# Optimization experiments

Measured on AMD Instinct MI355X. Metric: run time of the kernel, lower is better.

Reference implementation:

```python
import jax, jax.numpy as jnp
import numpy as np

EPS = 1e-5  # torch BatchNorm1d default eps


def setup_inputs() -> dict:
    key = jax.random.key(0)
    ks = jax.random.split(key, 12)
    B, D, H, R, T = 262144, 128, 64, 32, 8
    return {
        "x": jax.random.normal(ks[0], (B, D), dtype=jnp.float32),
        "t": jax.random.randint(ks[1], (B,), 0, T),
        # shared feature net: Linear(D->H), ReLU, BN(H) [eval mode], Dropout(eval=identity)
        "fw": jax.random.normal(ks[2], (H, D), dtype=jnp.float32) * 0.05,
        "fb": jax.random.normal(ks[3], (H,), dtype=jnp.float32) * 0.05,
        "f_gamma": jnp.ones((H,), jnp.float32),
        "f_beta": jnp.zeros((H,), jnp.float32),
        "f_mean": jax.random.normal(ks[4], (H,), dtype=jnp.float32) * 0.05,
        "f_var": jax.random.uniform(ks[5], (H,), minval=0.5, maxval=1.5),
        # T treatment heads, weights stacked on leading axis:
        # Linear(H->R), ReLU, BN(R), Dropout, Linear(R->1)
        "tw1": jax.random.normal(ks[6], (T, R, H), dtype=jnp.float32) * 0.05,
        "tb1": jax.random.normal(ks[7], (T, R), dtype=jnp.float32) * 0.05,
        "t_gamma": jnp.ones((T, R), jnp.float32),
        "t_beta": jnp.zeros((T, R), jnp.float32),
        "t_mean": jax.random.normal(ks[8], (T, R), dtype=jnp.float32) * 0.05,
        "t_var": jax.random.uniform(ks[9], (T, R), minval=0.5, maxval=1.5),
        "tw2": jax.random.normal(ks[10], (T, R), dtype=jnp.float32) * 0.05,  # [T,1,R] squeezed
        "tb2": jax.random.normal(ks[11], (T,), dtype=jnp.float32) * 0.05,
    }


def reference(x, t, fw, fb, f_gamma, f_beta, f_mean, f_var,
              tw1, tb1, t_gamma, t_beta, t_mean, t_var, tw2, tb2):
    # shared representation: Linear -> ReLU -> BN(eval) -> Dropout(identity)
    h = jax.nn.relu(x @ fw.T + fb)                                     # [B,H]
    h = f_gamma * (h - f_mean) * jax.lax.rsqrt(f_var + EPS) + f_beta   # [B,H]
    # run all T tiny heads densely, then select per-sample head (jit-friendly
    # equivalent of the boolean-mask gather/scatter loop; BN is eval-mode so
    # per-group masking and full-batch compute give identical math)
    z = jnp.einsum('bh,trh->btr', h, tw1) + tb1[None]                  # [B,T,R]
    z = jax.nn.relu(z)
    z = t_gamma[None] * (z - t_mean[None]) * jax.lax.rsqrt(t_var[None] + EPS) + t_beta[None]
    out_all = jnp.einsum('btr,tr->bt', z, tw2) + tb2[None]             # [B,T]
    pred = jnp.take_along_axis(out_all, t[:, None], axis=1)            # [B,1]
    return pred
```

## Files before the change

### kernel.cpp

```cpp
#include <hip/hip_runtime.h>
#include <hip/hip_bf16.h>
#include <cstdint>

#define EPS 1e-5f

typedef short bf16x8 __attribute__((ext_vector_type(8)));
typedef float f32x16 __attribute__((ext_vector_type(16)));
typedef unsigned int u32x4 __attribute__((ext_vector_type(4)));

#define WS_TW1S 0
#define WS_FWQ  8192
#define WS_TB1Q 12288
#define WS_W2Q  12544
#define WS_FBQ  12800
#define WS_C2   12864
#define WS_TOTAL 12872

static __device__ __forceinline__ unsigned short f2bf(float f) {
    unsigned int u = __float_as_uint(f);
    u += 0x7fffu + ((u >> 16) & 1u);
    return (unsigned short)(u >> 16);
}
static __device__ __forceinline__ unsigned pk_bf16(float lo, float hi) {
    unsigned l = (unsigned)(unsigned short)__builtin_bit_cast(unsigned short, __float2bfloat16(lo));
    unsigned h = (unsigned)(unsigned short)__builtin_bit_cast(unsigned short, __float2bfloat16(hi));
    return l | (h << 16);
}
static __device__ __forceinline__ short f2bf_fast(float f) {
    __hip_bfloat16 b = __float2bfloat16(f);
    return __builtin_bit_cast(short, b);
}

__global__ void tarnet_pre(
    const float* __restrict__ fw, const float* __restrict__ fb,
    const float* __restrict__ f_gamma, const float* __restrict__ f_beta,
    const float* __restrict__ f_mean,  const float* __restrict__ f_var,
    const float* __restrict__ tw1, const float* __restrict__ tb1,
    const float* __restrict__ t_gamma, const float* __restrict__ t_beta,
    const float* __restrict__ t_mean,  const float* __restrict__ t_var,
    const float* __restrict__ tw2, const float* __restrict__ tb2,
    float* __restrict__ ws)
{
    __shared__ float fs[64], fsh[64];
    const int i = threadIdx.x;
    if (i < 64) {
        float s = f_gamma[i] * rsqrtf(f_var[i] + EPS);
        fs[i]  = s;
        fsh[i] = f_beta[i] - f_mean[i] * s;
    }
    __syncthreads();

    unsigned short* tw1s_u = (unsigned short*)(ws + WS_TW1S);
    unsigned short* fwq_u  = (unsigned short*)(ws + WS_FWQ);

    const int t = i >> 5, r = i & 31;
    const int idx = t * 32 + r;
    {
        float tsc  = t_gamma[idx] * rsqrtf(t_var[idx] + EPS);
        float w2s  = tw2[idx] * tsc;
        float tb1s = tb1[idx];
        for (int j = 0; j < 64; ++j) {
            float w = tw1[idx * 64 + j];
            tb1s += w * fsh[j];
            int ht = j >> 5, qq = (j >> 3) & 3, h = (j >> 2) & 1, m = j & 3;
            int ks = ht * 2 + (qq >> 1);
            int ep = (qq & 1) * 4 + m;
            tw1s_u[(((t*4 + ks)*2 + h)*32 + r)*8 + ep] = f2bf(w * fs[j]);
        }
        int q  = ((r >> 3) << 2) | (r & 3);
        int hq = (r >> 2) & 1;
        ws[WS_TB1Q + (t*2 + hq)*16 + q] = tb1s;
        ws[WS_W2Q  + (t*2 + hq)*16 + q] = w2s;
    }
    if (r == 0) {
        float a = tb2[t];
        for (int rr = 0; rr < 32; ++rr) {
            int id2 = t*32 + rr;
            float ts2 = t_gamma[id2] * rsqrtf(t_var[id2] + EPS);
            a += tw2[id2] * (t_beta[id2] - ts2 * t_mean[id2]);
        }
        ws[WS_C2 + t] = a;
    }
    if (i < 64) {
        for (int k = 0; k < 128; ++k) {
            int ks = k >> 4, h = (k >> 3) & 1, jj = k & 7;
            fwq_u[(((ks*2 + h)*64) + i)*8 + jj] = f2bf(fw[i*128 + k]);
        }
        int ht = i >> 5, r32 = i & 31;
        int q  = ((r32 >> 3) << 2) | (r32 & 3);
        int hq = (r32 >> 2) & 1;
        ws[WS_FBQ + hq*32 + ht*16 + q] = fb[i];
    }
}

__global__ __launch_bounds__(256, 2) void tarnet_main(
    const float* __restrict__ x, const int* __restrict__ t_arr,
    const float* __restrict__ ws, float* __restrict__ out)
{
    __shared__ float smem[WS_TOTAL];
    {
        const uint4* src = (const uint4*)ws;
        uint4* dst = (uint4*)smem;
        for (int k = threadIdx.x; k < WS_TOTAL / 4; k += 256) dst[k] = src[k];
    }
    __syncthreads();

    const unsigned short* s_tw1s = (const unsigned short*)smem;
    const unsigned short* s_fwq  = (const unsigned short*)(smem + WS_FWQ);
    const float* s_tb1q = smem + WS_TB1Q;
    const float* s_w2q  = smem + WS_W2Q;
    const float* s_fbq  = smem + WS_FBQ;
    const float* s_c2   = smem + WS_C2;

    const int tid  = threadIdx.x;
    const int wave = tid >> 6, lane = tid & 63;
    const int ln31 = lane & 31, hi = lane >> 5;
    const int sbase = blockIdx.x * 256 + wave * 64;

    const int tsel0 = t_arr[sbase + ln31];
    const int tsel1 = t_arr[sbase + 32 + ln31];

    float4 xr[32];
    {
        const float4* xq0 = (const float4*)x + (size_t)(sbase + ln31) * 32 + hi * 2;
        const float4* xq1 = (const float4*)x + (size_t)(sbase + 32 + ln31) * 32 + hi * 2;
#pragma unroll
        for (int ks = 0; ks < 8; ++ks) {
            xr[2*ks]      = xq0[ks*4];
            xr[2*ks+1]    = xq0[ks*4 + 1];
            xr[16+2*ks]   = xq1[ks*4];
            xr[16+2*ks+1] = xq1[ks*4 + 1];
        }
    }
    bf16x8 xb[16];
#pragma unroll
    for (int i2 = 0; i2 < 16; ++i2) {
        float4 xa = xr[2*i2], xc = xr[2*i2+1];
        bf16x8 v;
        v[0] = f2bf_fast(xa.x); v[1] = f2bf_fast(xa.y);
        v[2] = f2bf_fast(xa.z); v[3] = f2bf_fast(xa.w);
        v[4] = f2bf_fast(xc.x); v[5] = f2bf_fast(xc.y);
        v[6] = f2bf_fast(xc.z); v[7] = f2bf_fast(xc.w);
        xb[i2] = v;
    }

    f32x16 acc[2][2];
    {
#pragma unroll
        for (int ht = 0; ht < 2; ++ht)
#pragma unroll
            for (int q = 0; q < 16; ++q) {
                float v = s_fbq[hi*32 + ht*16 + q];
                acc[0][ht][q] = v;
                acc[1][ht][q] = v;
            }
    }
#pragma unroll
    for (int ks = 0; ks < 8; ++ks) {
        bf16x8 wa0 = *(const bf16x8*)(s_fwq + (((ks*2 + hi)*64) + ln31     )*8);
        bf16x8 wa1 = *(const bf16x8*)(s_fwq + (((ks*2 + hi)*64) + ln31 + 32)*8);
        acc[0][0] = __builtin_amdgcn_mfma_f32_32x32x16_bf16(wa0, xb[ks],   acc[0][0], 0, 0, 0);
        acc[0][1] = __builtin_amdgcn_mfma_f32_32x32x16_bf16(wa1, xb[ks],   acc[0][1], 0, 0, 0);
        acc[1][0] = __builtin_amdgcn_mfma_f32_32x32x16_bf16(wa0, xb[8+ks], acc[1][0], 0, 0, 0);
        acc[1][1] = __builtin_amdgcn_mfma_f32_32x32x16_bf16(wa1, xb[8+ks], acc[1][1], 0, 0, 0);
    }

    bf16x8 hb[2][4];
#pragma unroll
    for (int st = 0; st < 2; ++st) {
        unsigned w0[2][4], w1[2][4];
#pragma unroll
        for (int ht = 0; ht < 2; ++ht)
#pragma unroll
            for (int qq = 0; qq < 4; ++qq) {
                float a0 = fmaxf(acc[st][ht][qq*4+0], 0.f);
                float a1 = fmaxf(acc[st][ht][qq*4+1], 0.f);
                float a2 = fmaxf(acc[st][ht][qq*4+2], 0.f);
                float a3 = fmaxf(acc[st][ht][qq*4+3], 0.f);
                w0[ht][qq] = pk_bf16(a0, a1);
                w1[ht][qq] = pk_bf16(a2, a3);
            }
#pragma unroll
        for (int ks = 0; ks < 4; ++ks) {
            const int ht = ks >> 1, qa = (ks & 1) * 2;
            u32x4 wv = {w0[ht][qa], w1[ht][qa], w0[ht][qa+1], w1[ht][qa+1]};
            hb[st][ks] = __builtin_bit_cast(bf16x8, wv);
        }
    }

    float out0 = 0.f, out1 = 0.f;
#pragma unroll 2
    for (int th = 0; th < 8; ++th) {
        bf16x8 aw[4];
#pragma unroll
        for (int ks = 0; ks < 4; ++ks)
            aw[ks] = *(const bf16x8*)(s_tw1s + (((th*4 + ks)*2 + hi)*32 + ln31)*8);
        const float* tbq = s_tb1q + (th*2 + hi)*16;
        const float* w2q = s_w2q  + (th*2 + hi)*16;
        const float c2t  = s_c2[th];
#pragma unroll
        for (int st = 0; st < 2; ++st) {
            f32x16 z;
#pragma unroll
            for (int q = 0; q < 16; ++q) z[q] = tbq[q];
            z = __builtin_amdgcn_mfma_f32_32x32x16_bf16(aw[0], hb[st][0], z, 0, 0, 0);
            z = __builtin_amdgcn_mfma_f32_32x32x16_bf16(aw[1], hb[st][1], z, 0, 0, 0);
            z = __builtin_amdgcn_mfma_f32_32x32x16_bf16(aw[2], hb[st][2], z, 0, 0, 0);
            z = __builtin_amdgcn_mfma_f32_32x32x16_bf16(aw[3], hb[st][3], z, 0, 0, 0);
            float p0 = 0.f, p1 = 0.f, p2 = 0.f, p3 = 0.f;
#pragma unroll
            for (int q = 0; q < 4; ++q) {
                p0 = fmaf(w2q[q],    fmaxf(z[q],    0.f), p0);
                p1 = fmaf(w2q[q+4],  fmaxf(z[q+4],  0.f), p1);
                p2 = fmaf(w2q[q+8],  fmaxf(z[q+8],  0.f), p2);
                p3 = fmaf(w2q[q+12], fmaxf(z[q+12], 0.f), p3);
            }
            float p = (p0 + p1) + (p2 + p3);
            p += __shfl_xor(p, 32);
            p += c2t;
            if (st == 0) out0 = (th == tsel0) ? p : out0;
            else         out1 = (th == tsel1) ? p : out1;
        }
    }
    out[sbase + lane] = hi ? out1 : out0;
}

extern "C" void kernel_launch(void* const* d_in, const int* in_sizes, int n_in,
                              void* d_out, int out_size, void* d_ws, size_t ws_size,
                              hipStream_t stream) {
    const float* x       = (const float*)d_in[0];
    const int*   t       = (const int*)  d_in[1];
    const float* fw      = (const float*)d_in[2];
    const float* fb      = (const float*)d_in[3];
    const float* f_gamma = (const float*)d_in[4];
    const float* f_beta  = (const float*)d_in[5];
    const float* f_mean  = (const float*)d_in[6];
    const float* f_var   = (const float*)d_in[7];
    const float* tw1     = (const float*)d_in[8];
    const float* tb1     = (const float*)d_in[9];
    const float* t_gamma = (const float*)d_in[10];
    const float* t_beta  = (const float*)d_in[11];
    const float* t_mean  = (const float*)d_in[12];
    const float* t_var   = (const float*)d_in[13];
    const float* tw2     = (const float*)d_in[14];
    const float* tb2     = (const float*)d_in[15];

    float* ws   = (float*)d_ws;
    float* outp = (float*)d_out;
    const int B = in_sizes[0] / 128;

    tarnet_pre<<<1, 256, 0, stream>>>(fw, fb, f_gamma, f_beta, f_mean, f_var,
                                      tw1, tb1, t_gamma, t_beta, t_mean, t_var,
                                      tw2, tb2, ws);
    tarnet_main<<<B / 256, 256, 0, stream>>>(x, t, ws, outp);
}
```

Baseline: 63.15 us.

## Stage x through swizzled LDS with coalesced loads, read weights from global

Replaces the per-lane strided x loads with block-wide coalesced float4 loads that convert to bf16 and store into an XOR-swizzled 64KB LDS tile, which the MFMA loop then reads back. The weight workspace is no longer copied to LDS; weights, biases and head vectors are read directly from global/cache. This aims to improve global load coalescing and register pressure, at the cost of a larger LDS footprint that may cap occupancy at two blocks per CU and of weight reads now going through the cache hierarchy.

```diff
diff --git a/kernel.cpp b/kernel.cpp
--- a/kernel.cpp
+++ b/kernel.cpp
@@ -14,21 +14,20 @@
 #define WS_W2Q  12544
 #define WS_FBQ  12800
 #define WS_C2   12864
-#define WS_TOTAL 12872
 
 static __device__ __forceinline__ unsigned short f2bf(float f) {
     unsigned int u = __float_as_uint(f);
     u += 0x7fffu + ((u >> 16) & 1u);
     return (unsigned short)(u >> 16);
 }
+static __device__ __forceinline__ short f2bf_fast(float f) {
+    __hip_bfloat16 b = __float2bfloat16(f);
+    return __builtin_bit_cast(short, b);
+}
 static __device__ __forceinline__ unsigned pk_bf16(float lo, float hi) {
     unsigned l = (unsigned)(unsigned short)__builtin_bit_cast(unsigned short, __float2bfloat16(lo));
     unsigned h = (unsigned)(unsigned short)__builtin_bit_cast(unsigned short, __float2bfloat16(hi));
     return l | (h << 16);
-}
-static __device__ __forceinline__ short f2bf_fast(float f) {
-    __hip_bfloat16 b = __float2bfloat16(f);
-    return __builtin_bit_cast(short, b);
 }
 
 __global__ void tarnet_pre(
@@ -97,72 +96,66 @@
     const float* __restrict__ x, const int* __restrict__ t_arr,
     const float* __restrict__ ws, float* __restrict__ out)
 {
-    __shared__ float smem[WS_TOTAL];
-    {
-        const uint4* src = (const uint4*)ws;
-        uint4* dst = (uint4*)smem;
-        for (int k = threadIdx.x; k < WS_TOTAL / 4; k += 256) dst[k] = src[k];
-    }
-    __syncthreads();
-
-    const unsigned short* s_tw1s = (const unsigned short*)smem;
-    const unsigned short* s_fwq  = (const unsigned short*)(smem + WS_FWQ);
-    const float* s_tb1q = smem + WS_TB1Q;
-    const float* s_w2q  = smem + WS_W2Q;
-    const float* s_fbq  = smem + WS_FBQ;
-    const float* s_c2   = smem + WS_C2;
+    __shared__ unsigned short x_lds_u[256 * 128];
+    char* xl = (char*)x_lds_u;
 
     const int tid  = threadIdx.x;
     const int wave = tid >> 6, lane = tid & 63;
     const int ln31 = lane & 31, hi = lane >> 5;
-    const int sbase = blockIdx.x * 256 + wave * 64;
-
-    const int tsel0 = t_arr[sbase + ln31];
-    const int tsel1 = t_arr[sbase + 32 + ln31];
-
-    float4 xr[32];
+    const int sbase = blockIdx.x * 256;
+
     {
-        const float4* xq0 = (const float4*)x + (size_t)(sbase + ln31) * 32 + hi * 2;
-        const float4* xq1 = (const float4*)x + (size_t)(sbase + 32 + ln31) * 32 + hi * 2;
-#pragma unroll
-        for (int ks = 0; ks < 8; ++ks) {
-            xr[2*ks]      = xq0[ks*4];
-            xr[2*ks+1]    = xq0[ks*4 + 1];
-            xr[16+2*ks]   = xq1[ks*4];
-            xr[16+2*ks+1] = xq1[ks*4 + 1];
-        }
-    }
-    bf16x8 xb[16];
-#pragma unroll
-    for (int i2 = 0; i2 < 16; ++i2) {
-        float4 xa = xr[2*i2], xc = xr[2*i2+1];
-        bf16x8 v;
-        v[0] = f2bf_fast(xa.x); v[1] = f2bf_fast(xa.y);
-        v[2] = f2bf_fast(xa.z); v[3] = f2bf_fast(xa.w);
-        v[4] = f2bf_fast(xc.x); v[5] = f2bf_fast(xc.y);
-        v[6] = f2bf_fast(xc.z); v[7] = f2bf_fast(xc.w);
-        xb[i2] = v;
-    }
+        const float4* xg = (const float4*)(x + (size_t)sbase * 128);
+#pragma unroll
+        for (int it = 0; it < 16; ++it) {
+            const int i = it * 256 + tid;
+            float4 a = xg[2*i], b = xg[2*i + 1];
+            bf16x8 v;
+            v[0] = f2bf_fast(a.x); v[1] = f2bf_fast(a.y);
+            v[2] = f2bf_fast(a.z); v[3] = f2bf_fast(a.w);
+            v[4] = f2bf_fast(b.x); v[5] = f2bf_fast(b.y);
+            v[6] = f2bf_fast(b.z); v[7] = f2bf_fast(b.w);
+            const int row = i >> 4, pcol = i & 15;
+            const int addr = row * 256 + ((pcol * 16) ^ ((row & 15) << 4));
+            *(bf16x8*)(xl + addr) = v;
+        }
+    }
+    __syncthreads();
+
+    const unsigned short* fwq_u  = (const unsigned short*)(ws + WS_FWQ);
+    const unsigned short* tw1s_u = (const unsigned short*)(ws + WS_TW1S);
+
+    const int tsel0 = t_arr[sbase + wave * 64 + ln31];
+    const int tsel1 = t_arr[sbase + wave * 64 + 32 + ln31];
+
+    const int srow0 = wave * 64 + ln31;
+    const int srow1 = srow0 + 32;
+    const int rb0 = srow0 * 256, xr0 = (srow0 & 15) << 4;
+    const int rb1 = srow1 * 256, xr1 = (srow1 & 15) << 4;
 
     f32x16 acc[2][2];
     {
+        const float* fbq = ws + WS_FBQ;
 #pragma unroll
         for (int ht = 0; ht < 2; ++ht)
 #pragma unroll
             for (int q = 0; q < 16; ++q) {
-                float v = s_fbq[hi*32 + ht*16 + q];
+                float v = fbq[hi*32 + ht*16 + q];
                 acc[0][ht][q] = v;
                 acc[1][ht][q] = v;
             }
     }
 #pragma unroll
     for (int ks = 0; ks < 8; ++ks) {
-        bf16x8 wa0 = *(const bf16x8*)(s_fwq + (((ks*2 + hi)*64) + ln31     )*8);
-        bf16x8 wa1 = *(const bf16x8*)(s_fwq + (((ks*2 + hi)*64) + ln31 + 32)*8);
-        acc[0][0] = __builtin_amdgcn_mfma_f32_32x32x16_bf16(wa0, xb[ks],   acc[0][0], 0, 0, 0);
-        acc[0][1] = __builtin_amdgcn_mfma_f32_32x32x16_bf16(wa1, xb[ks],   acc[0][1], 0, 0, 0);
-        acc[1][0] = __builtin_amdgcn_mfma_f32_32x32x16_bf16(wa0, xb[8+ks], acc[1][0], 0, 0, 0);
-        acc[1][1] = __builtin_amdgcn_mfma_f32_32x32x16_bf16(wa1, xb[8+ks], acc[1][1], 0, 0, 0);
+        bf16x8 wa0 = *(const bf16x8*)(fwq_u + (((ks*2 + hi)*64) + ln31     )*8);
+        bf16x8 wa1 = *(const bf16x8*)(fwq_u + (((ks*2 + hi)*64) + ln31 + 32)*8);
+        const int c = ks*32 + hi*16;
+        bf16x8 xf0 = *(const bf16x8*)(xl + rb0 + (c ^ xr0));
+        bf16x8 xf1 = *(const bf16x8*)(xl + rb1 + (c ^ xr1));
+        acc[0][0] = __builtin_amdgcn_mfma_f32_32x32x16_bf16(wa0, xf0, acc[0][0], 0, 0, 0);
+        acc[0][1] = __builtin_amdgcn_mfma_f32_32x32x16_bf16(wa1, xf0, acc[0][1], 0, 0, 0);
+        acc[1][0] = __builtin_amdgcn_mfma_f32_32x32x16_bf16(wa0, xf1, acc[1][0], 0, 0, 0);
+        acc[1][1] = __builtin_amdgcn_mfma_f32_32x32x16_bf16(wa1, xf1, acc[1][1], 0, 0, 0);
     }
 
     bf16x8 hb[2][4];
@@ -194,15 +187,19 @@
         bf16x8 aw[4];
 #pragma unroll
         for (int ks = 0; ks < 4; ++ks)
-            aw[ks] = *(const bf16x8*)(s_tw1s + (((th*4 + ks)*2 + hi)*32 + ln31)*8);
-        const float* tbq = s_tb1q + (th*2 + hi)*16;
-        const float* w2q = s_w2q  + (th*2 + hi)*16;
-        const float c2t  = s_c2[th];
+            aw[ks] = *(const bf16x8*)(tw1s_u + (((th*4 + ks)*2 + hi)*32 + ln31)*8);
+        float4 tb4[4], w24[4];
+#pragma unroll
+        for (int i2 = 0; i2 < 4; ++i2) {
+            tb4[i2] = ((const float4*)(ws + WS_TB1Q))[(th*2 + hi)*4 + i2];
+            w24[i2] = ((const float4*)(ws + WS_W2Q))[(th*2 + hi)*4 + i2];
+        }
+        const float c2t = ws[WS_C2 + th];
 #pragma unroll
         for (int st = 0; st < 2; ++st) {
             f32x16 z;
 #pragma unroll
-            for (int q = 0; q < 16; ++q) z[q] = tbq[q];
+            for (int q = 0; q < 16; ++q) z[q] = ((const float*)tb4)[q];
             z = __builtin_amdgcn_mfma_f32_32x32x16_bf16(aw[0], hb[st][0], z, 0, 0, 0);
             z = __builtin_amdgcn_mfma_f32_32x32x16_bf16(aw[1], hb[st][1], z, 0, 0, 0);
             z = __builtin_amdgcn_mfma_f32_32x32x16_bf16(aw[2], hb[st][2], z, 0, 0, 0);
@@ -210,10 +207,10 @@
             float p0 = 0.f, p1 = 0.f, p2 = 0.f, p3 = 0.f;
 #pragma unroll
             for (int q = 0; q < 4; ++q) {
-                p0 = fmaf(w2q[q],    fmaxf(z[q],    0.f), p0);
-                p1 = fmaf(w2q[q+4],  fmaxf(z[q+4],  0.f), p1);
-                p2 = fmaf(w2q[q+8],  fmaxf(z[q+8],  0.f), p2);
-                p3 = fmaf(w2q[q+12], fmaxf(z[q+12], 0.f), p3);
+                p0 = fmaf(((const float*)w24)[q],    fmaxf(z[q],    0.f), p0);
+                p1 = fmaf(((const float*)w24)[q+4],  fmaxf(z[q+4],  0.f), p1);
+                p2 = fmaf(((const float*)w24)[q+8],  fmaxf(z[q+8],  0.f), p2);
+                p3 = fmaf(((const float*)w24)[q+12], fmaxf(z[q+12], 0.f), p3);
             }
             float p = (p0 + p1) + (p2 + p3);
             p += __shfl_xor(p, 32);
@@ -222,7 +219,7 @@
             else         out1 = (th == tsel1) ? p : out1;
         }
     }
-    out[sbase + lane] = hi ? out1 : out0;
+    out[sbase + wave * 64 + lane] = hi ? out1 : out0;
 }
 
 extern "C" void kernel_launch(void* const* d_in, const int* in_sizes, int n_in,
```

Result: faster. 56.04 us (-11.3%).
